# Kernel tuning notes

Hardware: AMD Instinct MI355X
Metric: run time of the kernel (lower is better)

The kernel has to match this reference:

```python
import jax, jax.numpy as jnp
import numpy as np

D_MODEL = 1024
NUM_HEADS = 16
D_K = D_MODEL // NUM_HEADS
B, T = 4, 2048


def setup_inputs() -> dict:
    key = jax.random.key(0)
    ks = jax.random.split(key, 12)
    s = 0.02
    inp = {
        "query": jax.random.normal(ks[0], (B, T, D_MODEL), jnp.float32),
        "key": jax.random.normal(ks[1], (B, T, D_MODEL), jnp.float32),
        "value": jax.random.normal(ks[2], (B, T, D_MODEL), jnp.float32),
        "mask": jnp.tril(jnp.ones((T, T), jnp.int32))[None, None],  # [1,1,T,T] causal
        "Wq": jax.random.normal(ks[3], (D_MODEL, D_MODEL), jnp.float32) * s,
        "bq": jnp.zeros((D_MODEL,), jnp.float32),
        "Wk": jax.random.normal(ks[4], (D_MODEL, D_MODEL), jnp.float32) * s,
        "bk": jnp.zeros((D_MODEL,), jnp.float32),
        "Wv": jax.random.normal(ks[5], (D_MODEL, D_MODEL), jnp.float32) * s,
        "bv": jnp.zeros((D_MODEL,), jnp.float32),
        "Wo": jax.random.normal(ks[6], (D_MODEL, D_MODEL), jnp.float32) * s,
        "bo": jnp.zeros((D_MODEL,), jnp.float32),
    }
    return inp


def reference(query, key, value, mask, Wq, bq, Wk, bk, Wv, bv, Wo, bo):
    def split_heads(x):
        # [B,T,D] -> [B,H,T,Dk]
        return x.reshape(B, T, NUM_HEADS, D_K).transpose(0, 2, 1, 3)

    q = split_heads(query @ Wq.T + bq)
    k = split_heads(key @ Wk.T + bk)
    v = split_heads(value @ Wv.T + bv)

    scale = jnp.sqrt(jnp.asarray(D_K, q.dtype))
    scores = jnp.einsum("bhqd,bhkd->bhqk", q, k) / scale  # [B,H,T,T]
    scores = jnp.where(mask == 0, jnp.asarray(-1e9, scores.dtype), scores)
    attn = jax.nn.softmax(scores, axis=-1)
    out = jnp.einsum("bhqk,bhkd->bhqd", attn, v)
    out = out.transpose(0, 2, 1, 3).reshape(B, T, D_MODEL)
    return out @ Wo.T + bo
```

## Files before the change

### kernel.cpp

```cpp
#include <hip/hip_runtime.h>
#include <hip/hip_bf16.h>

#define D_MODEL 1024
#define NHEADS  16
#define DK      64
#define BATCH   4
#define SEQ     2048
#define M_TOT   (BATCH * SEQ)

typedef __attribute__((ext_vector_type(8)))  __bf16 bf16x8;
typedef __attribute__((ext_vector_type(4)))  float  f32x4;
typedef __attribute__((ext_vector_type(16))) float  f32x16;
typedef unsigned short ushort_t;

static __device__ __forceinline__ unsigned int f2bf(float f) {
    union { float f; unsigned int i; } v; v.f = f;
    unsigned int x = v.i;
    return (x + 0x7fffu + ((x >> 16) & 1u)) >> 16;
}

static __device__ __forceinline__ void gl16(const void* g, void* lds_generic) {
    __attribute__((address_space(1))) void* gp =
        (__attribute__((address_space(1))) void*)(unsigned long long)g;
    __attribute__((address_space(3))) void* lp =
        (__attribute__((address_space(3))) void*)(unsigned int)(unsigned long long)lds_generic;
    __builtin_amdgcn_global_load_lds(gp, lp, 16, 0, 0);
}

__global__ __launch_bounds__(256) void cvt_in3(
    const float* __restrict__ i0, const float* __restrict__ i1,
    const float* __restrict__ i2,
    ushort_t* __restrict__ o0, ushort_t* __restrict__ o1,
    ushort_t* __restrict__ o2, int n8)
{
    const float* in; ushort_t* out;
    switch (blockIdx.y) {
        case 0: in = i0; out = o0; break;
        case 1: in = i1; out = o1; break;
        default: in = i2; out = o2; break;
    }
    int i = blockIdx.x * blockDim.x + threadIdx.x;
    if (i >= n8) return;
    const float4* p = (const float4*)in + (size_t)i * 2;
    float4 a = p[0], b = p[1];
    uint4 o;
    o.x = f2bf(a.x) | (f2bf(a.y) << 16);
    o.y = f2bf(a.z) | (f2bf(a.w) << 16);
    o.z = f2bf(b.x) | (f2bf(b.y) << 16);
    o.w = f2bf(b.z) | (f2bf(b.w) << 16);
    *((uint4*)out + i) = o;
}

__global__ __launch_bounds__(256) void cvt_w4(
    const float* __restrict__ w0, const float* __restrict__ w1,
    const float* __restrict__ w2, const float* __restrict__ w3,
    ushort_t* __restrict__ o0, ushort_t* __restrict__ o1,
    ushort_t* __restrict__ o2, ushort_t* __restrict__ o3, int n8)
{
    const float* w; ushort_t* o;
    switch (blockIdx.y) {
        case 0: w = w0; o = o0; break;
        case 1: w = w1; o = o1; break;
        case 2: w = w2; o = o2; break;
        default: w = w3; o = o3; break;
    }
    int i = blockIdx.x * blockDim.x + threadIdx.x;
    if (i >= n8) return;
    const float4* p = (const float4*)w + (size_t)i * 2;
    float4 a = p[0], b = p[1];
    uint4 u;
    u.x = f2bf(a.x) | (f2bf(a.y) << 16);
    u.y = f2bf(a.z) | (f2bf(a.w) << 16);
    u.z = f2bf(b.x) | (f2bf(b.y) << 16);
    u.w = f2bf(b.z) | (f2bf(b.w) << 16);
    *((uint4*)o + i) = u;
}

__global__ __launch_bounds__(512) void gemm_nt_bias(
    const ushort_t* __restrict__ A0, const ushort_t* __restrict__ A1,
    const ushort_t* __restrict__ A2,
    const ushort_t* __restrict__ B0, const ushort_t* __restrict__ B1,
    const ushort_t* __restrict__ B2,
    const float* __restrict__ b0, const float* __restrict__ b1,
    const float* __restrict__ b2,
    void* __restrict__ O0, void* __restrict__ O1, void* __restrict__ O2,
    int mode)
{
    const int z = blockIdx.z;
    const ushort_t* A  = (z == 0) ? A0 : (z == 1) ? A1 : A2;
    const ushort_t* Bt = (z == 0) ? B0 : (z == 1) ? B1 : B2;
    const float* bias  = (z == 0) ? b0 : (z == 1) ? b1 : b2;
    void* OutV         = (z == 0) ? O0 : (z == 1) ? O1 : O2;
    const float oscale = (mode == 1 && z == 0) ? 0.18033688f : 1.0f;

    __shared__ ushort_t sA[2][128 * 64];
    __shared__ ushort_t sB[2][128 * 64];
    const int K    = 1024;
    const int tid  = threadIdx.x;
    const int lane = tid & 63;
    const int wave = tid >> 6;

    const int flat = (int)blockIdx.x + 8 * (int)blockIdx.y;
    const int nf   = (flat & 7) * 64 + (flat >> 3);
    const int m0   = (nf >> 3) * 128;
    const int n0   = (nf & 7) * 128;

    const int wrow = (wave >> 2) * 64;
    const int wcol = (wave & 3) * 32;
    const int l15  = lane & 15;
    const int quad = lane >> 4;
    const int swz  = l15 & 7;

    size_t aoffs[2], boffs[2];
#pragma unroll
    for (int i = 0; i < 2; i++) {
        int c = tid + 512 * i;
        int row = c >> 3;
        int ch  = (c & 7) ^ (row & 7);
        aoffs[i] = (size_t)(m0 + row) * K + ch * 8;
        boffs[i] = (size_t)(n0 + row) * K + ch * 8;
    }

    f32x4 acc[4][2];
#pragma unroll
    for (int i = 0; i < 4; i++)
#pragma unroll
        for (int j = 0; j < 2; j++)
#pragma unroll
            for (int r = 0; r < 4; r++) acc[i][j][r] = 0.0f;

    auto stage = [&](int buf, int kt) {
#pragma unroll
        for (int i = 0; i < 2; i++) {
            int c = tid + 512 * i;
            gl16(A + aoffs[i] + kt, &sA[buf][c * 8]);
            gl16(Bt + boffs[i] + kt, &sB[buf][c * 8]);
        }
    };

    stage(0, 0);
    asm volatile("s_waitcnt vmcnt(0)");
    __syncthreads();
    int cur = 0;

    for (int kt = 0; kt < K; kt += 64) {
        if (kt + 64 < K) stage(cur ^ 1, kt + 64);

#pragma unroll
        for (int kk = 0; kk < 2; kk++) {
            bf16x8 afr[4], bfr[2];
            const int chp = ((kk * 4 + quad) ^ swz) * 8;
#pragma unroll
            for (int i = 0; i < 4; i++)
                afr[i] = *(const bf16x8*)(&sA[cur][(wrow + i * 16 + l15) * 64 + chp]);
#pragma unroll
            for (int j = 0; j < 2; j++)
                bfr[j] = *(const bf16x8*)(&sB[cur][(wcol + j * 16 + l15) * 64 + chp]);
#pragma unroll
            for (int i = 0; i < 4; i++)
#pragma unroll
                for (int j = 0; j < 2; j++)
                    acc[i][j] = __builtin_amdgcn_mfma_f32_16x16x32_bf16(
                        afr[i], bfr[j], acc[i][j], 0, 0, 0);
        }

        asm volatile("s_waitcnt vmcnt(0)");
        __syncthreads();
        cur ^= 1;
    }

    if (mode == 1 && z == 2) {
#pragma unroll
        for (int j = 0; j < 2; j++) {
            int col  = n0 + wcol + j * 16 + l15;
            float bv = bias[col];
            int h = col >> 6, dk = col & 63;
#pragma unroll
            for (int i = 0; i < 4; i++) {
                int row0 = m0 + wrow + i * 16 + quad * 4;
                int b = row0 >> 11, t0 = row0 & 2047;
                ushort_t pk[4];
#pragma unroll
                for (int r = 0; r < 4; r++)
                    pk[r] = (ushort_t)f2bf(acc[i][j][r] + bv);
                *(uint2*)&((ushort_t*)OutV)[((size_t)(b * 16 + h) * 64 + dk) * SEQ + t0] =
                    *(const uint2*)pk;
            }
        }
        return;
    }

#pragma unroll
    for (int j = 0; j < 2; j++) {
        int col  = n0 + wcol + j * 16 + l15;
        float bv = bias[col];
#pragma unroll
        for (int i = 0; i < 4; i++) {
#pragma unroll
            for (int r = 0; r < 4; r++) {
                int row = m0 + wrow + i * 16 + quad * 4 + r;
                float o = (acc[i][j][r] + bv) * oscale;
                if (mode == 0) {
                    ((ushort_t*)OutV)[(size_t)row * 1024 + col] = (ushort_t)f2bf(o);
                } else if (mode == 1) {
                    int b = row >> 11, t = row & 2047;
                    int h = col >> 6,  dk = col & 63;
                    ((ushort_t*)OutV)[((size_t)(b * 16 + h) * 2048 + t) * 64 + dk] =
                        (ushort_t)f2bf(o);
                } else {
                    ((float*)OutV)[(size_t)row * 1024 + col] = o;
                }
            }
        }
    }
}

__global__ __launch_bounds__(256, 2) void attn_causal(
    const ushort_t* __restrict__ Q,
    const ushort_t* __restrict__ Km,
    const ushort_t* __restrict__ Vt,
    ushort_t* __restrict__ O)
{
    __shared__ ushort_t sK[2][64 * 64];
    __shared__ ushort_t sVt[2][64 * 64];

    const int tid  = threadIdx.x;
    const int lane = tid & 63;
    const int wave = tid >> 6;
    const int l31  = lane & 31;
    const int hi   = lane >> 5;
    const int bh   = blockIdx.x;
    const int qtile = 15 - (int)blockIdx.y;
    const size_t base = (size_t)bh * SEQ * 64;

    size_t ksrc[2], vsrc[2];
#pragma unroll
    for (int i = 0; i < 2; i++) {
        int c  = tid + 256 * i;
        int kr = c >> 3, kc = (c & 7) ^ (kr & 7);
        ksrc[i] = base + (size_t)kr * 64 + kc * 8;
        int vr = c >> 3, vc = (c & 7) ^ (vr & 7);
        vsrc[i] = base + (size_t)vr * SEQ + vc * 8;
    }

    bf16x8 qfr[4];
    f32x16 oacc[2];
    float  ls[4];

#pragma unroll
    for (int j = 0; j < 2; j++)
#pragma unroll
        for (int r = 0; r < 16; r++) oacc[j][r] = 0.0f;
#pragma unroll
    for (int r = 0; r < 4; r++) ls[r] = 0.0f;

    {
        const size_t qrow = base + (size_t)(qtile * 128 + wave * 32 + l31) * 64;
#pragma unroll
        for (int kk = 0; kk < 4; kk++)
            qfr[kk] = *(const bf16x8*)&Q[qrow + kk * 16 + hi * 8];
    }

    auto stage = [&](int buf, int s) {
        const size_t ko = (size_t)s * 64 * 64;
        const size_t vo = (size_t)s * 64;
#pragma unroll
        for (int i = 0; i < 2; i++) {
            int c = tid + 256 * i;
            gl16(Km + ksrc[i] + ko, &sK[buf][c * 8]);
            gl16(Vt + vsrc[i] + vo, &sVt[buf][c * 8]);
        }
    };

    auto compute = [&](int cur, int s64) {
        const ushort_t* kb_ = &sK[cur][0];
        const ushort_t* vb_ = &sVt[cur][0];
        const int kv0   = s64 * 64;
        const int qgmin = qtile * 128 + wave * 32;
        const int qg    = qgmin + l31;

        f32x16 sacc[2];
#pragma unroll
        for (int b = 0; b < 2; b++) {
            if (kv0 + b * 32 > qgmin + 31) continue;
#pragma unroll
            for (int r = 0; r < 16; r++) sacc[b][r] = 0.0f;
            const int krow = b * 32 + l31;
            const int ksw  = krow & 7;
            __builtin_amdgcn_s_setprio(1);
#pragma unroll
            for (int kk = 0; kk < 4; kk++) {
                bf16x8 afr = *(const bf16x8*)&kb_[krow * 64 + (((kk * 2 + hi) ^ ksw) * 8)];
                sacc[b] = __builtin_amdgcn_mfma_f32_32x32x16_bf16(afr, qfr[kk], sacc[b], 0, 0, 0);
            }
            __builtin_amdgcn_s_setprio(0);
        }

#pragma unroll
        for (int b = 0; b < 2; b++) {
            if (kv0 + b * 32 > qgmin + 31) continue;
            const bool maskb = (kv0 + b * 32 + 31) > qgmin;

            float p[16];
#pragma unroll
            for (int r = 0; r < 16; r++) {
                float v = sacc[b][r];
                if (maskb) {
                    int kvg = kv0 + b * 32 + (r & 3) + 8 * (r >> 2) + 4 * hi;
                    if (kvg > qg) v = -INFINITY;
                }
                float e = __builtin_amdgcn_exp2f(v);
                p[r] = e;
                ls[r & 3] += e;
            }

            unsigned w[8];
#pragma unroll
            for (int t = 0; t < 4; t++) {
                asm("v_cvt_pk_bf16_f32 %0, %1, %2"
                    : "=v"(w[2 * t]) : "v"(p[4 * t]), "v"(p[4 * t + 1]));
                asm("v_cvt_pk_bf16_f32 %0, %1, %2"
                    : "=v"(w[2 * t + 1]) : "v"(p[4 * t + 2]), "v"(p[4 * t + 3]));
            }

#pragma unroll
            for (int kb = 0; kb < 2; kb++) {
                unsigned aA = w[kb * 4 + 0], bA = w[kb * 4 + 2];
                unsigned aB = w[kb * 4 + 1], bB = w[kb * 4 + 3];
                asm("v_permlane32_swap_b32 %0, %1" : "+v"(aA), "+v"(bA));
                asm("v_permlane32_swap_b32 %0, %1" : "+v"(aB), "+v"(bB));
                union { unsigned u[4]; bf16x8 v8; } fr;
                fr.u[0] = aA; fr.u[1] = aB; fr.u[2] = bA; fr.u[3] = bB;
                __builtin_amdgcn_s_setprio(1);
#pragma unroll
                for (int j = 0; j < 2; j++) {
                    const int vrow = j * 32 + l31;
                    bf16x8 bfr = *(const bf16x8*)&vb_[
                        vrow * 64 + (((b * 4 + kb * 2 + hi) ^ (vrow & 7)) * 8)];
                    oacc[j] = __builtin_amdgcn_mfma_f32_32x32x16_bf16(
                        fr.v8, bfr, oacc[j], 0, 0, 0);
                }
                __builtin_amdgcn_s_setprio(0);
            }
        }
    };

    const int send = 2 * qtile + 1;
    stage(0, 0);
    asm volatile("s_waitcnt vmcnt(0)");
    __syncthreads();
    int cur = 0;
    for (int u = 0; u <= send; ++u) {
        if (u < send) stage(cur ^ 1, u + 1);
        compute(cur, u);
        asm volatile("s_waitcnt vmcnt(0)");
        __syncthreads();
        cur ^= 1;
    }

    const int ob = bh >> 4, oh = bh & 15;
    {
        float lsum = (ls[0] + ls[1]) + (ls[2] + ls[3]);
        float tot = lsum + __shfl_xor(lsum, 32);
        float inv = 1.0f / tot;
#pragma unroll
        for (int r = 0; r < 16; r++) {
            int qloc = (r & 3) + 8 * (r >> 2) + 4 * hi;
            float invr = __shfl(inv, qloc);
            int qg2 = qtile * 128 + wave * 32 + qloc;
#pragma unroll
            for (int j = 0; j < 2; j++) {
                O[((size_t)(ob * SEQ) + qg2) * 1024 + oh * 64 + j * 32 + l31] =
                    (ushort_t)f2bf(oacc[j][r] * invr);
            }
        }
    }
}

extern "C" void kernel_launch(void* const* d_in, const int* in_sizes, int n_in,
                              void* d_out, int out_size, void* d_ws, size_t ws_size,
                              hipStream_t stream) {
    const float* q_in = (const float*)d_in[0];
    const float* k_in = (const float*)d_in[1];
    const float* v_in = (const float*)d_in[2];
    const float* Wq = (const float*)d_in[4];
    const float* bq = (const float*)d_in[5];
    const float* Wk = (const float*)d_in[6];
    const float* bk = (const float*)d_in[7];
    const float* Wv = (const float*)d_in[8];
    const float* bv = (const float*)d_in[9];
    const float* Wo = (const float*)d_in[10];
    const float* bo = (const float*)d_in[11];

    ushort_t* ws = (ushort_t*)d_ws;
    const size_t TEN = (size_t)M_TOT * D_MODEL;
    const size_t WEL = (size_t)D_MODEL * D_MODEL;
    ushort_t* tmp = ws;
    ushort_t* WqB = ws + TEN;
    ushort_t* WkB = WqB + WEL;
    ushort_t* WvB = WkB + WEL;
    ushort_t* WoB = WvB + WEL;
    ushort_t* qw  = WoB + WEL;
    ushort_t* kw  = qw + TEN;
    ushort_t* vw  = kw + TEN;
    ushort_t* ow  = vw + TEN;
    ushort_t* vstage = (ushort_t*)d_out;

    dim3 bb(256);
    dim3 bg(512);
    const int n8_in = (int)(TEN / 8);
    const int n8_w  = (int)(WEL / 8);

    cvt_w4<<<dim3(n8_w / 256, 4), bb, 0, stream>>>(Wq, Wk, Wv, Wo, WqB, WkB, WvB, WoB, n8_w);
    cvt_in3<<<dim3(n8_in / 256, 3), bb, 0, stream>>>(q_in, k_in, v_in, tmp, ow, vstage, n8_in);

    gemm_nt_bias<<<dim3(D_MODEL / 128, M_TOT / 128, 3), bg, 0, stream>>>(
        tmp, ow, vstage, WqB, WkB, WvB, bq, bk, bv, qw, kw, vw, 1);

    attn_causal<<<dim3(BATCH * NHEADS, 16), bb, 0, stream>>>(qw, kw, vw, ow);

    gemm_nt_bias<<<dim3(D_MODEL / 128, M_TOT / 128, 1), bg, 0, stream>>>(
        ow, ow, ow, WoB, WoB, WoB, bo, bo, bo, d_out, d_out, d_out, 2);
}
```

Before: 317.2 us.

## Fuse fp32-to-bf16 conversion into GEMM tile loaders, drop convert kernels

Removes the separate input and weight conversion kernels; the projection GEMM now loads fp32 activations and weights through registers, packs them to bf16 with v_cvt_pk_bf16_f32, and writes them to LDS after the MFMA step. This avoids the extra global write and reread of bf16 copies and two kernel launches. In exchange, fp32 tiles are fetched repeatedly across blocks at twice the byte width and staging goes through registers instead of async LDS loads, which may reduce overlap.

```diff
diff --git a/kernel.cpp b/kernel.cpp
--- a/kernel.cpp
+++ b/kernel.cpp
@@ -27,70 +27,31 @@
     __builtin_amdgcn_global_load_lds(gp, lp, 16, 0, 0);
 }
 
-__global__ __launch_bounds__(256) void cvt_in3(
-    const float* __restrict__ i0, const float* __restrict__ i1,
-    const float* __restrict__ i2,
-    ushort_t* __restrict__ o0, ushort_t* __restrict__ o1,
-    ushort_t* __restrict__ o2, int n8)
-{
-    const float* in; ushort_t* out;
-    switch (blockIdx.y) {
-        case 0: in = i0; out = o0; break;
-        case 1: in = i1; out = o1; break;
-        default: in = i2; out = o2; break;
-    }
-    int i = blockIdx.x * blockDim.x + threadIdx.x;
-    if (i >= n8) return;
-    const float4* p = (const float4*)in + (size_t)i * 2;
-    float4 a = p[0], b = p[1];
-    uint4 o;
-    o.x = f2bf(a.x) | (f2bf(a.y) << 16);
-    o.y = f2bf(a.z) | (f2bf(a.w) << 16);
-    o.z = f2bf(b.x) | (f2bf(b.y) << 16);
-    o.w = f2bf(b.z) | (f2bf(b.w) << 16);
-    *((uint4*)out + i) = o;
-}
-
-__global__ __launch_bounds__(256) void cvt_w4(
-    const float* __restrict__ w0, const float* __restrict__ w1,
-    const float* __restrict__ w2, const float* __restrict__ w3,
-    ushort_t* __restrict__ o0, ushort_t* __restrict__ o1,
-    ushort_t* __restrict__ o2, ushort_t* __restrict__ o3, int n8)
-{
-    const float* w; ushort_t* o;
-    switch (blockIdx.y) {
-        case 0: w = w0; o = o0; break;
-        case 1: w = w1; o = o1; break;
-        case 2: w = w2; o = o2; break;
-        default: w = w3; o = o3; break;
-    }
-    int i = blockIdx.x * blockDim.x + threadIdx.x;
-    if (i >= n8) return;
-    const float4* p = (const float4*)w + (size_t)i * 2;
-    float4 a = p[0], b = p[1];
+static __device__ __forceinline__ uint4 pack8(float4 lo, float4 hi) {
     uint4 u;
-    u.x = f2bf(a.x) | (f2bf(a.y) << 16);
-    u.y = f2bf(a.z) | (f2bf(a.w) << 16);
-    u.z = f2bf(b.x) | (f2bf(b.y) << 16);
-    u.w = f2bf(b.z) | (f2bf(b.w) << 16);
-    *((uint4*)o + i) = u;
+    asm("v_cvt_pk_bf16_f32 %0, %1, %2" : "=v"(u.x) : "v"(lo.x), "v"(lo.y));
+    asm("v_cvt_pk_bf16_f32 %0, %1, %2" : "=v"(u.y) : "v"(lo.z), "v"(lo.w));
+    asm("v_cvt_pk_bf16_f32 %0, %1, %2" : "=v"(u.z) : "v"(hi.x), "v"(hi.y));
+    asm("v_cvt_pk_bf16_f32 %0, %1, %2" : "=v"(u.w) : "v"(hi.z), "v"(hi.w));
+    return u;
 }
 
 __global__ __launch_bounds__(512) void gemm_nt_bias(
-    const ushort_t* __restrict__ A0, const ushort_t* __restrict__ A1,
-    const ushort_t* __restrict__ A2,
-    const ushort_t* __restrict__ B0, const ushort_t* __restrict__ B1,
-    const ushort_t* __restrict__ B2,
+    const void* __restrict__ A0v, const void* __restrict__ A1v,
+    const void* __restrict__ A2v,
+    const float* __restrict__ W0, const float* __restrict__ W1,
+    const float* __restrict__ W2,
     const float* __restrict__ b0, const float* __restrict__ b1,
     const float* __restrict__ b2,
     void* __restrict__ O0, void* __restrict__ O1, void* __restrict__ O2,
     int mode)
 {
     const int z = blockIdx.z;
-    const ushort_t* A  = (z == 0) ? A0 : (z == 1) ? A1 : A2;
-    const ushort_t* Bt = (z == 0) ? B0 : (z == 1) ? B1 : B2;
-    const float* bias  = (z == 0) ? b0 : (z == 1) ? b1 : b2;
-    void* OutV         = (z == 0) ? O0 : (z == 1) ? O1 : O2;
+    const float* Af = (const float*)((z == 0) ? A0v : (z == 1) ? A1v : A2v);
+    const ushort_t* Ab = (const ushort_t*)A0v;
+    const float* Wf = (z == 0) ? W0 : (z == 1) ? W1 : W2;
+    const float* bias = (z == 0) ? b0 : (z == 1) ? b1 : b2;
+    void* OutV = (z == 0) ? O0 : (z == 1) ? O1 : O2;
     const float oscale = (mode == 1 && z == 0) ? 0.18033688f : 1.0f;
 
     __shared__ ushort_t sA[2][128 * 64];
@@ -112,9 +73,11 @@
     const int swz  = l15 & 7;
 
     size_t aoffs[2], boffs[2];
+    int cidx[2];
 #pragma unroll
     for (int i = 0; i < 2; i++) {
         int c = tid + 512 * i;
+        cidx[i] = c;
         int row = c >> 3;
         int ch  = (c & 7) ^ (row & 7);
         aoffs[i] = (size_t)(m0 + row) * K + ch * 8;
@@ -129,22 +92,37 @@
 #pragma unroll
             for (int r = 0; r < 4; r++) acc[i][j][r] = 0.0f;
 
-    auto stage = [&](int buf, int kt) {
-#pragma unroll
-        for (int i = 0; i < 2; i++) {
-            int c = tid + 512 * i;
-            gl16(A + aoffs[i] + kt, &sA[buf][c * 8]);
-            gl16(Bt + boffs[i] + kt, &sB[buf][c * 8]);
-        }
-    };
-
-    stage(0, 0);
+#pragma unroll
+    for (int i = 0; i < 2; i++) {
+        if (mode == 1) {
+            const float4* pa = (const float4*)(Af + aoffs[i]);
+            *(uint4*)&sA[0][cidx[i] * 8] = pack8(pa[0], pa[1]);
+        } else {
+            gl16(Ab + aoffs[i], &sA[0][cidx[i] * 8]);
+        }
+        const float4* pb = (const float4*)(Wf + boffs[i]);
+        *(uint4*)&sB[0][cidx[i] * 8] = pack8(pb[0], pb[1]);
+    }
     asm volatile("s_waitcnt vmcnt(0)");
     __syncthreads();
     int cur = 0;
 
     for (int kt = 0; kt < K; kt += 64) {
-        if (kt + 64 < K) stage(cur ^ 1, kt + 64);
+        const bool nxt = (kt + 64 < K);
+        float4 aL[2], aH[2], bL[2], bH[2];
+        if (nxt) {
+#pragma unroll
+            for (int i = 0; i < 2; i++) {
+                if (mode == 1) {
+                    const float4* pa = (const float4*)(Af + aoffs[i] + kt + 64);
+                    aL[i] = pa[0]; aH[i] = pa[1];
+                } else {
+                    gl16(Ab + aoffs[i] + kt + 64, &sA[cur ^ 1][cidx[i] * 8]);
+                }
+                const float4* pb = (const float4*)(Wf + boffs[i] + kt + 64);
+                bL[i] = pb[0]; bH[i] = pb[1];
+            }
+        }
 
 #pragma unroll
         for (int kk = 0; kk < 2; kk++) {
@@ -162,6 +140,15 @@
                 for (int j = 0; j < 2; j++)
                     acc[i][j] = __builtin_amdgcn_mfma_f32_16x16x32_bf16(
                         afr[i], bfr[j], acc[i][j], 0, 0, 0);
+        }
+
+        if (nxt) {
+#pragma unroll
+            for (int i = 0; i < 2; i++) {
+                if (mode == 1)
+                    *(uint4*)&sA[cur ^ 1][cidx[i] * 8] = pack8(aL[i], aH[i]);
+                *(uint4*)&sB[cur ^ 1][cidx[i] * 8] = pack8(bL[i], bH[i]);
+            }
         }
 
         asm volatile("s_waitcnt vmcnt(0)");
@@ -200,9 +187,7 @@
             for (int r = 0; r < 4; r++) {
                 int row = m0 + wrow + i * 16 + quad * 4 + r;
                 float o = (acc[i][j][r] + bv) * oscale;
-                if (mode == 0) {
-                    ((ushort_t*)OutV)[(size_t)row * 1024 + col] = (ushort_t)f2bf(o);
-                } else if (mode == 1) {
+                if (mode == 1) {
                     int b = row >> 11, t = row & 2047;
                     int h = col >> 6,  dk = col & 63;
                     ((ushort_t*)OutV)[((size_t)(b * 16 + h) * 2048 + t) * 64 + dk] =
@@ -394,31 +379,18 @@
 
     ushort_t* ws = (ushort_t*)d_ws;
     const size_t TEN = (size_t)M_TOT * D_MODEL;
-    const size_t WEL = (size_t)D_MODEL * D_MODEL;
-    ushort_t* tmp = ws;
-    ushort_t* WqB = ws + TEN;
-    ushort_t* WkB = WqB + WEL;
-    ushort_t* WvB = WkB + WEL;
-    ushort_t* WoB = WvB + WEL;
-    ushort_t* qw  = WoB + WEL;
-    ushort_t* kw  = qw + TEN;
-    ushort_t* vw  = kw + TEN;
-    ushort_t* ow  = vw + TEN;
-    ushort_t* vstage = (ushort_t*)d_out;
-
-    dim3 bb(256);
+    ushort_t* qw = ws;
+    ushort_t* kw = qw + TEN;
+    ushort_t* vw = kw + TEN;
+    ushort_t* ow = vw + TEN;
+
     dim3 bg(512);
-    const int n8_in = (int)(TEN / 8);
-    const int n8_w  = (int)(WEL / 8);
-
-    cvt_w4<<<dim3(n8_w / 256, 4), bb, 0, stream>>>(Wq, Wk, Wv, Wo, WqB, WkB, WvB, WoB, n8_w);
-    cvt_in3<<<dim3(n8_in / 256, 3), bb, 0, stream>>>(q_in, k_in, v_in, tmp, ow, vstage, n8_in);
-
-    gemm_nt_bias<<<dim3(D_MODEL / 128, M_TOT / 128, 3), bg, 0, stream>>>(
-        tmp, ow, vstage, WqB, WkB, WvB, bq, bk, bv, qw, kw, vw, 1);
-
-    attn_causal<<<dim3(BATCH * NHEADS, 16), bb, 0, stream>>>(qw, kw, vw, ow);
-
-    gemm_nt_bias<<<dim3(D_MODEL / 128, M_TOT / 128, 1), bg, 0, stream>>>(
-        ow, ow, ow, WoB, WoB, WoB, bo, bo, bo, d_out, d_out, d_out, 2);
-}
+
+    gemm_nt_bias<<<dim3(8, 64, 3), bg, 0, stream>>>(
+        q_in, k_in, v_in, Wq, Wk, Wv, bq, bk, bv, qw, kw, vw, 1);
+
+    attn_causal<<<dim3(BATCH * NHEADS, 16), dim3(256), 0, stream>>>(qw, kw, vw, ow);
+
+    gemm_nt_bias<<<dim3(8, 64, 1), bg, 0, stream>>>(
+        ow, ow, ow, Wo, Wo, Wo, bo, bo, bo, d_out, d_out, d_out, 2);
+}
```

Result: slower. 369.2 us (+16.4%).

## Fuse fp32-to-bf16 input conversion into QKV projection GEMM

Applied to the files above, without the earlier changes.

Removes the separate pass that converts the query, key and value activations to bf16. The QKV GEMM now stages fp32 A tiles straight into LDS with an XOR swizzle and converts them to bf16 in registers using v_cvt_pk_bf16_f32 before the MFMA. The single mode-switched GEMM is split into specialised gemm_qkv and gemm_out kernels. This drops one kernel launch and a full write and re-read of three bf16 activation tensors, at the cost of twice the LDS footprint and global traffic for the A tiles, plus extra conversion ALU work inside the GEMM loop.

```diff
diff --git a/kernel.cpp b/kernel.cpp
--- a/kernel.cpp
+++ b/kernel.cpp
@@ -27,28 +27,13 @@
     __builtin_amdgcn_global_load_lds(gp, lp, 16, 0, 0);
 }
 
-__global__ __launch_bounds__(256) void cvt_in3(
-    const float* __restrict__ i0, const float* __restrict__ i1,
-    const float* __restrict__ i2,
-    ushort_t* __restrict__ o0, ushort_t* __restrict__ o1,
-    ushort_t* __restrict__ o2, int n8)
-{
-    const float* in; ushort_t* out;
-    switch (blockIdx.y) {
-        case 0: in = i0; out = o0; break;
-        case 1: in = i1; out = o1; break;
-        default: in = i2; out = o2; break;
-    }
-    int i = blockIdx.x * blockDim.x + threadIdx.x;
-    if (i >= n8) return;
-    const float4* p = (const float4*)in + (size_t)i * 2;
-    float4 a = p[0], b = p[1];
-    uint4 o;
-    o.x = f2bf(a.x) | (f2bf(a.y) << 16);
-    o.y = f2bf(a.z) | (f2bf(a.w) << 16);
-    o.z = f2bf(b.x) | (f2bf(b.y) << 16);
-    o.w = f2bf(b.z) | (f2bf(b.w) << 16);
-    *((uint4*)out + i) = o;
+static __device__ __forceinline__ uint4 pack8(f32x4 lo, f32x4 hi) {
+    uint4 u;
+    asm("v_cvt_pk_bf16_f32 %0, %1, %2" : "=v"(u.x) : "v"(lo[0]), "v"(lo[1]));
+    asm("v_cvt_pk_bf16_f32 %0, %1, %2" : "=v"(u.y) : "v"(lo[2]), "v"(lo[3]));
+    asm("v_cvt_pk_bf16_f32 %0, %1, %2" : "=v"(u.z) : "v"(hi[0]), "v"(hi[1]));
+    asm("v_cvt_pk_bf16_f32 %0, %1, %2" : "=v"(u.w) : "v"(hi[2]), "v"(hi[3]));
+    return u;
 }
 
 __global__ __launch_bounds__(256) void cvt_w4(
@@ -76,23 +61,158 @@
     *((uint4*)o + i) = u;
 }
 
-__global__ __launch_bounds__(512) void gemm_nt_bias(
-    const ushort_t* __restrict__ A0, const ushort_t* __restrict__ A1,
-    const ushort_t* __restrict__ A2,
+__global__ __launch_bounds__(512) void gemm_qkv(
+    const float* __restrict__ A0, const float* __restrict__ A1,
+    const float* __restrict__ A2,
     const ushort_t* __restrict__ B0, const ushort_t* __restrict__ B1,
     const ushort_t* __restrict__ B2,
     const float* __restrict__ b0, const float* __restrict__ b1,
     const float* __restrict__ b2,
-    void* __restrict__ O0, void* __restrict__ O1, void* __restrict__ O2,
-    int mode)
+    ushort_t* __restrict__ O0, ushort_t* __restrict__ O1,
+    ushort_t* __restrict__ O2)
 {
     const int z = blockIdx.z;
-    const ushort_t* A  = (z == 0) ? A0 : (z == 1) ? A1 : A2;
+    const float* Af    = (z == 0) ? A0 : (z == 1) ? A1 : A2;
     const ushort_t* Bt = (z == 0) ? B0 : (z == 1) ? B1 : B2;
     const float* bias  = (z == 0) ? b0 : (z == 1) ? b1 : b2;
-    void* OutV         = (z == 0) ? O0 : (z == 1) ? O1 : O2;
-    const float oscale = (mode == 1 && z == 0) ? 0.18033688f : 1.0f;
-
+    ushort_t* Out      = (z == 0) ? O0 : (z == 1) ? O1 : O2;
+    const float oscale = (z == 0) ? 0.18033688f : 1.0f;
+
+    __shared__ float    sA[2][128 * 64];
+    __shared__ ushort_t sB[2][128 * 64];
+    const int K    = 1024;
+    const int tid  = threadIdx.x;
+    const int lane = tid & 63;
+    const int wave = tid >> 6;
+
+    const int flat = (int)blockIdx.x + 8 * (int)blockIdx.y;
+    const int nf   = (flat & 7) * 64 + (flat >> 3);
+    const int m0   = (nf >> 3) * 128;
+    const int n0   = (nf & 7) * 128;
+
+    const int wrow = (wave >> 2) * 64;
+    const int wcol = (wave & 3) * 32;
+    const int l15  = lane & 15;
+    const int quad = lane >> 4;
+
+    size_t aoffs[4];
+#pragma unroll
+    for (int i = 0; i < 4; i++) {
+        int c = tid + 512 * i;
+        int row = c >> 4;
+        int ch  = (c & 15) ^ (row & 15);
+        aoffs[i] = (size_t)(m0 + row) * K + ch * 4;
+    }
+    size_t boffs[2];
+#pragma unroll
+    for (int i = 0; i < 2; i++) {
+        int c = tid + 512 * i;
+        int row = c >> 3;
+        int ch  = (c & 7) ^ (row & 7);
+        boffs[i] = (size_t)(n0 + row) * K + ch * 8;
+    }
+
+    f32x4 acc[4][2];
+#pragma unroll
+    for (int i = 0; i < 4; i++)
+#pragma unroll
+        for (int j = 0; j < 2; j++)
+#pragma unroll
+            for (int r = 0; r < 4; r++) acc[i][j][r] = 0.0f;
+
+    auto stage = [&](int buf, int kt) {
+#pragma unroll
+        for (int i = 0; i < 4; i++)
+            gl16(Af + aoffs[i] + kt, &sA[buf][(tid + 512 * i) * 4]);
+#pragma unroll
+        for (int i = 0; i < 2; i++)
+            gl16(Bt + boffs[i] + kt, &sB[buf][(tid + 512 * i) * 8]);
+    };
+
+    stage(0, 0);
+    asm volatile("s_waitcnt vmcnt(0)");
+    __syncthreads();
+    int cur = 0;
+
+    for (int kt = 0; kt < K; kt += 64) {
+        if (kt + 64 < K) stage(cur ^ 1, kt + 64);
+
+#pragma unroll
+        for (int kk = 0; kk < 2; kk++) {
+            const int chp8 = kk * 4 + quad;
+            bf16x8 afr[4], bfr[2];
+#pragma unroll
+            for (int i = 0; i < 4; i++) {
+                int r = wrow + i * 16 + l15;
+                const float* ar = &sA[cur][r * 64];
+                f32x4 a0 = *(const f32x4*)&ar[((2 * chp8) ^ l15) * 4];
+                f32x4 a1 = *(const f32x4*)&ar[((2 * chp8 + 1) ^ l15) * 4];
+                union { uint4 u; bf16x8 v; } cvt;
+                cvt.u = pack8(a0, a1);
+                afr[i] = cvt.v;
+            }
+#pragma unroll
+            for (int j = 0; j < 2; j++)
+                bfr[j] = *(const bf16x8*)(&sB[cur][(wcol + j * 16 + l15) * 64 +
+                                                   ((chp8 ^ (l15 & 7)) * 8)]);
+#pragma unroll
+            for (int i = 0; i < 4; i++)
+#pragma unroll
+                for (int j = 0; j < 2; j++)
+                    acc[i][j] = __builtin_amdgcn_mfma_f32_16x16x32_bf16(
+                        afr[i], bfr[j], acc[i][j], 0, 0, 0);
+        }
+
+        asm volatile("s_waitcnt vmcnt(0)");
+        __syncthreads();
+        cur ^= 1;
+    }
+
+    if (z == 2) {
+#pragma unroll
+        for (int j = 0; j < 2; j++) {
+            int col  = n0 + wcol + j * 16 + l15;
+            float bv = bias[col];
+            int h = col >> 6, dk = col & 63;
+#pragma unroll
+            for (int i = 0; i < 4; i++) {
+                int row0 = m0 + wrow + i * 16 + quad * 4;
+                int b = row0 >> 11, t0 = row0 & 2047;
+                ushort_t pk[4];
+#pragma unroll
+                for (int r = 0; r < 4; r++)
+                    pk[r] = (ushort_t)f2bf(acc[i][j][r] + bv);
+                *(uint2*)&Out[((size_t)(b * 16 + h) * 64 + dk) * SEQ + t0] =
+                    *(const uint2*)pk;
+            }
+        }
+        return;
+    }
+
+#pragma unroll
+    for (int j = 0; j < 2; j++) {
+        int col  = n0 + wcol + j * 16 + l15;
+        float bv = bias[col];
+        int h = col >> 6, dk = col & 63;
+#pragma unroll
+        for (int i = 0; i < 4; i++) {
+#pragma unroll
+            for (int r = 0; r < 4; r++) {
+                int row = m0 + wrow + i * 16 + quad * 4 + r;
+                float o = (acc[i][j][r] + bv) * oscale;
+                int b = row >> 11, t = row & 2047;
+                Out[((size_t)(b * 16 + h) * 2048 + t) * 64 + dk] = (ushort_t)f2bf(o);
+            }
+        }
+    }
+}
+
+__global__ __launch_bounds__(512) void gemm_out(
+    const ushort_t* __restrict__ A,
+    const ushort_t* __restrict__ Bt,
+    const float* __restrict__ bias,
+    float* __restrict__ Out)
+{
     __shared__ ushort_t sA[2][128 * 64];
     __shared__ ushort_t sB[2][128 * 64];
     const int K    = 1024;
@@ -169,27 +289,6 @@
         cur ^= 1;
     }
 
-    if (mode == 1 && z == 2) {
-#pragma unroll
-        for (int j = 0; j < 2; j++) {
-            int col  = n0 + wcol + j * 16 + l15;
-            float bv = bias[col];
-            int h = col >> 6, dk = col & 63;
-#pragma unroll
-            for (int i = 0; i < 4; i++) {
-                int row0 = m0 + wrow + i * 16 + quad * 4;
-                int b = row0 >> 11, t0 = row0 & 2047;
-                ushort_t pk[4];
-#pragma unroll
-                for (int r = 0; r < 4; r++)
-                    pk[r] = (ushort_t)f2bf(acc[i][j][r] + bv);
-                *(uint2*)&((ushort_t*)OutV)[((size_t)(b * 16 + h) * 64 + dk) * SEQ + t0] =
-                    *(const uint2*)pk;
-            }
-        }
-        return;
-    }
-
 #pragma unroll
     for (int j = 0; j < 2; j++) {
         int col  = n0 + wcol + j * 16 + l15;
@@ -199,17 +298,7 @@
 #pragma unroll
             for (int r = 0; r < 4; r++) {
                 int row = m0 + wrow + i * 16 + quad * 4 + r;
-                float o = (acc[i][j][r] + bv) * oscale;
-                if (mode == 0) {
-                    ((ushort_t*)OutV)[(size_t)row * 1024 + col] = (ushort_t)f2bf(o);
-                } else if (mode == 1) {
-                    int b = row >> 11, t = row & 2047;
-                    int h = col >> 6,  dk = col & 63;
-                    ((ushort_t*)OutV)[((size_t)(b * 16 + h) * 2048 + t) * 64 + dk] =
-                        (ushort_t)f2bf(o);
-                } else {
-                    ((float*)OutV)[(size_t)row * 1024 + col] = o;
-                }
+                Out[(size_t)row * 1024 + col] = acc[i][j][r] + bv;
             }
         }
     }
@@ -395,8 +484,7 @@
     ushort_t* ws = (ushort_t*)d_ws;
     const size_t TEN = (size_t)M_TOT * D_MODEL;
     const size_t WEL = (size_t)D_MODEL * D_MODEL;
-    ushort_t* tmp = ws;
-    ushort_t* WqB = ws + TEN;
+    ushort_t* WqB = ws;
     ushort_t* WkB = WqB + WEL;
     ushort_t* WvB = WkB + WEL;
     ushort_t* WoB = WvB + WEL;
@@ -404,21 +492,16 @@
     ushort_t* kw  = qw + TEN;
     ushort_t* vw  = kw + TEN;
     ushort_t* ow  = vw + TEN;
-    ushort_t* vstage = (ushort_t*)d_out;
-
-    dim3 bb(256);
-    dim3 bg(512);
-    const int n8_in = (int)(TEN / 8);
-    const int n8_w  = (int)(WEL / 8);
-
-    cvt_w4<<<dim3(n8_w / 256, 4), bb, 0, stream>>>(Wq, Wk, Wv, Wo, WqB, WkB, WvB, WoB, n8_w);
-    cvt_in3<<<dim3(n8_in / 256, 3), bb, 0, stream>>>(q_in, k_in, v_in, tmp, ow, vstage, n8_in);
-
-    gemm_nt_bias<<<dim3(D_MODEL / 128, M_TOT / 128, 3), bg, 0, stream>>>(
-        tmp, ow, vstage, WqB, WkB, WvB, bq, bk, bv, qw, kw, vw, 1);
-
-    attn_causal<<<dim3(BATCH * NHEADS, 16), bb, 0, stream>>>(qw, kw, vw, ow);
-
-    gemm_nt_bias<<<dim3(D_MODEL / 128, M_TOT / 128, 1), bg, 0, stream>>>(
-        ow, ow, ow, WoB, WoB, WoB, bo, bo, bo, d_out, d_out, d_out, 2);
-}
+
+    const int n8_w = (int)(WEL / 8);
+
+    cvt_w4<<<dim3(n8_w / 256, 4), dim3(256), 0, stream>>>(
+        Wq, Wk, Wv, Wo, WqB, WkB, WvB, WoB, n8_w);
+
+    gemm_qkv<<<dim3(8, 64, 3), dim3(512), 0, stream>>>(
+        q_in, k_in, v_in, WqB, WkB, WvB, bq, bk, bv, qw, kw, vw);
+
+    attn_causal<<<dim3(BATCH * NHEADS, 16), dim3(256), 0, stream>>>(qw, kw, vw, ow);
+
+    gemm_out<<<dim3(8, 64, 1), dim3(512), 0, stream>>>(ow, WoB, bo, (float*)d_out);
+}
```

Measured after the change: 372.3 us. +17.4%, slower.
